# Kernel optimization log

Hardware: AMD Instinct MI355X
Metric: run time of the kernel (lower is better)

The kernel has to match this reference:

```python
import jax, jax.numpy as jnp
import numpy as np

IMG_H, IMG_W = 800, 1216
STRIDE = 16
SIZES = (128.0, 256.0, 512.0)
RATIOS = (0.5, 1.0, 2.0)
NMS_THRESH = 0.7
MIN_SIZE = 16.0
PRE_NMS = 6000   # testing mode
POST_NMS = 300   # testing mode


def _base_anchors():
    # torchvision-style: ratio = h/w, anchors centered at origin, xyxy
    base = []
    for s in SIZES:
        for r in RATIOS:
            hr = np.sqrt(r)
            w, h = s / hr, s * hr
            base.append([-w / 2.0, -h / 2.0, w / 2.0, h / 2.0])
    return jnp.asarray(np.array(base, dtype=np.float32))  # [A,4]


def _anchors(H, W):
    base = _base_anchors()                                  # [A,4]
    sx = jnp.arange(W, dtype=jnp.float32) * STRIDE
    sy = jnp.arange(H, dtype=jnp.float32) * STRIDE
    shift_x, shift_y = jnp.meshgrid(sx, sy)                 # [H,W] each
    shifts = jnp.stack([shift_x, shift_y, shift_x, shift_y], axis=-1)
    # row-major over (h, w), anchors innermost -> matches permute(0,2,3,1) layout
    return (shifts.reshape(-1, 1, 4) + base[None]).reshape(-1, 4)  # [H*W*A,4]


def _conv(x, w, b, pad):
    y = jax.lax.conv_general_dilated(x, w, (1, 1), pad,
                                     dimension_numbers=('NCHW', 'OIHW', 'NCHW'))
    return y + b[None, :, None, None]


def _decode(deltas, anchors):
    wa = anchors[:, 2] - anchors[:, 0]
    ha = anchors[:, 3] - anchors[:, 1]
    cxa = anchors[:, 0] + 0.5 * wa
    cya = anchors[:, 1] + 0.5 * ha
    cx = deltas[:, 0] * wa + cxa
    cy = deltas[:, 1] * ha + cya
    w = jnp.exp(deltas[:, 2]) * wa
    h = jnp.exp(deltas[:, 3]) * ha
    return jnp.stack([cx - 0.5 * w, cy - 0.5 * h, cx + 0.5 * w, cy + 0.5 * h], axis=-1)


def _nms(boxes, scores):
    # boxes: [N,4] sorted by descending score; greedy IoU-suppression NMS
    N = boxes.shape[0]
    areas = (boxes[:, 2] - boxes[:, 0]) * (boxes[:, 3] - boxes[:, 1])

    def body(i, st):
        sup, kidx, kval = st
        avail = jnp.where(sup, -jnp.inf, scores)
        j = jnp.argmax(avail)
        valid = avail[j] > -jnp.inf
        b = boxes[j]
        ix1 = jnp.maximum(b[0], boxes[:, 0])
        iy1 = jnp.maximum(b[1], boxes[:, 1])
        ix2 = jnp.minimum(b[2], boxes[:, 2])
        iy2 = jnp.minimum(b[3], boxes[:, 3])
        inter = jnp.clip(ix2 - ix1, 0.0) * jnp.clip(iy2 - iy1, 0.0)
        union = areas[j] + areas - inter
        iou = jnp.where(union > 0, inter / union, 0.0)
        sup2 = (sup | (iou > NMS_THRESH)).at[j].set(True)
        sup = jnp.where(valid, sup2, sup.at[j].set(True))
        return sup, kidx.at[i].set(j), kval.at[i].set(valid)

    sup0 = jnp.zeros((N,), jnp.bool_)
    _, kidx, kval = jax.lax.fori_loop(
        0, POST_NMS, body,
        (sup0, jnp.zeros((POST_NMS,), jnp.int32), jnp.zeros((POST_NMS,), jnp.bool_)))
    # fixed-size output [POST_NMS,4]; invalid slots zeroed
    return boxes[kidx] * kval[:, None].astype(boxes.dtype)


def setup_inputs() -> dict:
    key = jax.random.key(0)
    ks = jax.random.split(key, 4)
    return {
        'features': jax.random.normal(ks[0], (8, 512, 50, 76), jnp.float32),
        'conv_w': 0.01 * jax.random.normal(ks[1], (512, 512, 3, 3), jnp.float32),
        'conv_b': jnp.zeros((512,), jnp.float32),
        'cls_w': 0.01 * jax.random.normal(ks[2], (9, 512, 1, 1), jnp.float32),
        'cls_b': jnp.zeros((9,), jnp.float32),
        'box_w': 0.01 * jax.random.normal(ks[3], (36, 512, 1, 1), jnp.float32),
        'box_b': jnp.zeros((36,), jnp.float32),
    }


def reference(features, conv_w, conv_b, cls_w, cls_b, box_w, box_b):
    B, _, H, W = features.shape
    t = jax.nn.relu(_conv(features, conv_w, conv_b, 'SAME'))
    obj = _conv(t, cls_w, cls_b, 'VALID')                     # [B,A,H,W]
    objectness = jnp.transpose(obj, (0, 2, 3, 1)).reshape(B, -1)        # [B,N]
    bd = _conv(t, box_w, box_b, 'VALID')                      # [B,4A,H,W]
    bbox_deltas = jnp.transpose(bd, (0, 2, 3, 1)).reshape(B, -1, 4)     # [B,N,4]
    anchors = _anchors(H, W)                                  # [N,4]

    def per_image(scores, deltas):
        props = _decode(deltas, anchors)
        props = jnp.stack([jnp.clip(props[:, 0], 0.0, IMG_W),
                           jnp.clip(props[:, 1], 0.0, IMG_H),
                           jnp.clip(props[:, 2], 0.0, IMG_W),
                           jnp.clip(props[:, 3], 0.0, IMG_H)], axis=-1)
        keep = ((props[:, 2] - props[:, 0]) >= MIN_SIZE) & \
               ((props[:, 3] - props[:, 1]) >= MIN_SIZE)
        s = jnp.where(keep, scores, -jnp.inf)  # small boxes never selected
        top_s, top_i = jax.lax.top_k(s, PRE_NMS)
        return _nms(props[top_i], top_s)

    proposals = jax.vmap(per_image)(objectness, bbox_deltas)  # [B,POST_NMS,4]
    return proposals, objectness, bbox_deltas
```

## Files before the change

### kernel.cpp

```cpp
#include <hip/hip_runtime.h>
#include <stdint.h>
#include <math.h>

typedef unsigned int u32;
typedef unsigned long long u64;
typedef double d4 __attribute__((ext_vector_type(4)));
typedef _Float16 h8 __attribute__((ext_vector_type(8)));
typedef float f32x16 __attribute__((ext_vector_type(16)));

#define NPX    3800
#define NANCH  34200
#define NSEL   6000
#define NOUT   300
#define NPXP   4160

#define OFF_T        0ull
#define OFF_WTH      62259200ull
#define OFF_WTL      66977792ull
#define OFF_BOXES    71696384ull
#define OFF_ITEMS    76073984ull
#define OFF_FSPH     78262784ull
#define OFF_FSPL     112341504ull
#define WS_NEED_F16  146551296ull
#define OFF_PART     OFF_FSPH
#define WS_NEED_SPLITK (OFF_PART + 43776000ull)

#define GLL16(gsrc, ldst) \
    __builtin_amdgcn_global_load_lds((const __attribute__((address_space(1))) void*)(gsrc), \
                                     (__attribute__((address_space(3))) void*)(ldst), 16, 0, 0)

__global__ __launch_bounds__(256) void zero_kernel(float4* __restrict__ p, unsigned n) {
    unsigned i = blockIdx.x * 256u + threadIdx.x;
    const unsigned stride = gridDim.x * 256u;
    const float4 z = make_float4(0.f, 0.f, 0.f, 0.f);
    for (; i < n; i += stride) p[i] = z;
}

__global__ __launch_bounds__(256) void wsplit_kernel(const float* __restrict__ cw,
                                                     _Float16* __restrict__ wh,
                                                     _Float16* __restrict__ wl) {
    int o = blockIdx.x * 256 + threadIdx.x;
    if (o >= 9 * 512 * 512) return;
    int ci = o & 511;
    int co = (o >> 9) & 511;
    int kk = o >> 18;
    float v = cw[(((co << 9) + ci) * 9) + kk] * 1024.0f;
    _Float16 h = (_Float16)v;
    float r = v - (float)h;
    wh[o] = h;
    wl[o] = (_Float16)r;
}

__global__ __launch_bounds__(256) void fsplit_kernel(const float* __restrict__ feat,
                                                     _Float16* __restrict__ fh,
                                                     _Float16* __restrict__ fl) {
    const int b = blockIdx.z, ci0 = blockIdx.y << 5, p0 = blockIdx.x << 6;
    const int tid = threadIdx.x;
    __shared__ __align__(16) _Float16 shh[64][32];
    __shared__ __align__(16) _Float16 shl[64][32];
    {
        const int r = tid >> 3, xg = tid & 7;
        const int p = p0 + (xg << 3);
        float v[8];
        if (p < NPX) {
            const float* sp = feat + ((size_t)(b * 512 + ci0 + r)) * NPX + p;
            #pragma unroll
            for (int j = 0; j < 8; ++j) v[j] = sp[j];
        } else {
            #pragma unroll
            for (int j = 0; j < 8; ++j) v[j] = 0.f;
        }
        #pragma unroll
        for (int j = 0; j < 8; ++j) {
            float s = v[j] * 512.0f;
            _Float16 h = (_Float16)s;
            float rr = s - (float)h;
            shh[(xg << 3) + j][r] = h;
            shl[(xg << 3) + j][r] = (_Float16)rr;
        }
    }
    __syncthreads();
    {
        const int px = tid >> 2, cg = tid & 3;
        const int p = p0 + px;
        if (p < NPX) {
            const int yy = p / 76, xx = p - yy * 76;
            const size_t dst = ((size_t)b * NPXP + (size_t)((yy + 1) * 80 + xx + 2)) * 512
                             + ci0 + (cg << 3);
            *(h8*)(fh + dst) = *(const h8*)&shh[px][cg << 3];
            *(h8*)(fl + dst) = *(const h8*)&shl[px][cg << 3];
        }
    }
}

__global__ __launch_bounds__(512, 2) void conv3x3_f16_kernel(
    const _Float16* __restrict__ fh, const _Float16* __restrict__ fl,
    const _Float16* __restrict__ wh, const _Float16* __restrict__ wl,
    const float* __restrict__ bias, float* __restrict__ t)
{
    const int id  = blockIdx.x;
    const int b   = id & 7;
    const int g   = id >> 3;
    const int co0 = (g >> 4) << 7;
    const int pt0 = (g & 15) << 8;
    const int tid = threadIdx.x;
    const int w   = tid >> 6;
    const int l   = tid & 63;
    const int wm  = w >> 2, wn = w & 3;
    const int ln  = l & 31, lk = l >> 5;

    __shared__ __align__(16) _Float16 S[5][24][512];

    const _Float16* sb[3];
    u32 ldof[3];
    bool isA[3];
    const long long fbase = (long long)b * NPXP + pt0;
    #pragma unroll
    for (int i = 0; i < 3; ++i) {
        const int ti = w * 3 + i;
        ldof[i] = (u32)(ti * 1024 + l * 16);
        isA[i] = (ti < 8);
        if (ti < 8) {
            const int mt = ti >> 1, hl = ti & 1;
            sb[i] = (hl ? wl : wh) + ((long long)(co0 + (mt << 5) + ln) << 9) + (lk << 3);
        } else {
            const int tj = ti - 8, nt = tj >> 1, hl = tj & 1;
            sb[i] = (hl ? fl : fh) + ((fbase + (nt << 5) + ln) << 9) + (lk << 3);
        }
    }
    char* lbase = (char*)&S[0][0][0];

    auto stage = [&](int q, int slot) {
        const int kk  = q >> 5;
        const int ci0 = (q & 31) << 4;
        const long long offA = ((long long)kk << 18) + ci0;
        const int kd = (kk * 11) >> 5;
        const int s  = kd * 77 + kk - 81;
        const long long offB = ((long long)s << 9) + ci0;
        char* ld = lbase + slot * 24576;
        #pragma unroll
        for (int i = 0; i < 3; ++i) {
            const long long off = isA[i] ? offA : offB;
            GLL16(sb[i] + off, ld + ldof[i]);
        }
    };

    f32x16 acc[2][2], l2[2][2];
    #pragma unroll
    for (int i = 0; i < 2; ++i)
        #pragma unroll
        for (int j = 0; j < 2; ++j)
            #pragma unroll
            for (int gg = 0; gg < 16; ++gg) { acc[i][j][gg] = 0.0f; l2[i][j][gg] = 0.0f; }

    const int ao = l << 3;

    auto readFrags = [&](int slot, h8* Ah, h8* Al, h8* Bh, h8* Bl) {
        const _Float16* Sq = (const _Float16*)(lbase + slot * 24576);
        #pragma unroll
        for (int i = 0; i < 2; ++i) {
            const int mt = (wm << 1) + i, nt = (wn << 1) + i;
            Ah[i] = *(const h8*)(Sq + (((mt << 1) + 0) << 9) + ao);
            Al[i] = *(const h8*)(Sq + (((mt << 1) + 1) << 9) + ao);
            Bh[i] = *(const h8*)(Sq + ((8 + (nt << 1) + 0) << 9) + ao);
            Bl[i] = *(const h8*)(Sq + ((8 + (nt << 1) + 1) << 9) + ao);
        }
    };

    stage(0, 0); stage(1, 1); stage(2, 2);
    asm volatile("s_waitcnt vmcnt(3)" ::: "memory");
    __builtin_amdgcn_sched_barrier(0);
    __builtin_amdgcn_s_barrier();

    int s0 = 0;
    for (int F = 0; F < 144; ++F) {
        const int q0 = F << 1;
        int s1 = s0 + 1; if (s1 >= 5) s1 -= 5;
        int s3 = s0 + 3; if (s3 >= 5) s3 -= 5;
        int s4 = s0 + 4; if (s4 >= 5) s4 -= 5;
        if (q0 + 3 < 288) stage(q0 + 3, s3);
        if (q0 + 4 < 288) stage(q0 + 4, s4);

        h8 A0h[2], A0l[2], B0h[2], B0l[2];
        h8 A1h[2], A1l[2], B1h[2], B1l[2];
        readFrags(s0, A0h, A0l, B0h, B0l);
        __builtin_amdgcn_s_setprio(1);
        acc[0][0] = __builtin_amdgcn_mfma_f32_32x32x16_f16(A0h[0], B0h[0], acc[0][0], 0, 0, 0);
        acc[0][0] = __builtin_amdgcn_mfma_f32_32x32x16_f16(A0h[0], B0l[0], acc[0][0], 0, 0, 0);
        acc[0][0] = __builtin_amdgcn_mfma_f32_32x32x16_f16(A0l[0], B0h[0], acc[0][0], 0, 0, 0);
        acc[0][1] = __builtin_amdgcn_mfma_f32_32x32x16_f16(A0h[0], B0h[1], acc[0][1], 0, 0, 0);
        acc[0][1] = __builtin_amdgcn_mfma_f32_32x32x16_f16(A0h[0], B0l[1], acc[0][1], 0, 0, 0);
        acc[0][1] = __builtin_amdgcn_mfma_f32_32x32x16_f16(A0l[0], B0h[1], acc[0][1], 0, 0, 0);
        __builtin_amdgcn_s_setprio(0);
        readFrags(s1, A1h, A1l, B1h, B1l);
        __builtin_amdgcn_s_setprio(1);
        acc[1][0] = __builtin_amdgcn_mfma_f32_32x32x16_f16(A0h[1], B0h[0], acc[1][0], 0, 0, 0);
        acc[1][0] = __builtin_amdgcn_mfma_f32_32x32x16_f16(A0h[1], B0l[0], acc[1][0], 0, 0, 0);
        acc[1][0] = __builtin_amdgcn_mfma_f32_32x32x16_f16(A0l[1], B0h[0], acc[1][0], 0, 0, 0);
        acc[1][1] = __builtin_amdgcn_mfma_f32_32x32x16_f16(A0h[1], B0h[1], acc[1][1], 0, 0, 0);
        acc[1][1] = __builtin_amdgcn_mfma_f32_32x32x16_f16(A0h[1], B0l[1], acc[1][1], 0, 0, 0);
        acc[1][1] = __builtin_amdgcn_mfma_f32_32x32x16_f16(A0l[1], B0h[1], acc[1][1], 0, 0, 0);
        acc[0][0] = __builtin_amdgcn_mfma_f32_32x32x16_f16(A1h[0], B1h[0], acc[0][0], 0, 0, 0);
        acc[0][0] = __builtin_amdgcn_mfma_f32_32x32x16_f16(A1h[0], B1l[0], acc[0][0], 0, 0, 0);
        acc[0][0] = __builtin_amdgcn_mfma_f32_32x32x16_f16(A1l[0], B1h[0], acc[0][0], 0, 0, 0);
        acc[0][1] = __builtin_amdgcn_mfma_f32_32x32x16_f16(A1h[0], B1h[1], acc[0][1], 0, 0, 0);
        acc[0][1] = __builtin_amdgcn_mfma_f32_32x32x16_f16(A1h[0], B1l[1], acc[0][1], 0, 0, 0);
        acc[0][1] = __builtin_amdgcn_mfma_f32_32x32x16_f16(A1l[0], B1h[1], acc[0][1], 0, 0, 0);
        acc[1][0] = __builtin_amdgcn_mfma_f32_32x32x16_f16(A1h[1], B1h[0], acc[1][0], 0, 0, 0);
        acc[1][0] = __builtin_amdgcn_mfma_f32_32x32x16_f16(A1h[1], B1l[0], acc[1][0], 0, 0, 0);
        acc[1][0] = __builtin_amdgcn_mfma_f32_32x32x16_f16(A1l[1], B1h[0], acc[1][0], 0, 0, 0);
        acc[1][1] = __builtin_amdgcn_mfma_f32_32x32x16_f16(A1h[1], B1h[1], acc[1][1], 0, 0, 0);
        acc[1][1] = __builtin_amdgcn_mfma_f32_32x32x16_f16(A1h[1], B1l[1], acc[1][1], 0, 0, 0);
        acc[1][1] = __builtin_amdgcn_mfma_f32_32x32x16_f16(A1l[1], B1h[1], acc[1][1], 0, 0, 0);
        __builtin_amdgcn_s_setprio(0);

        if (((q0 + 1) & 7) == 7) {
            #pragma unroll
            for (int i = 0; i < 2; ++i)
                #pragma unroll
                for (int j = 0; j < 2; ++j) {
                    l2[i][j] += acc[i][j];
                    #pragma unroll
                    for (int gg = 0; gg < 16; ++gg) acc[i][j][gg] = 0.0f;
                }
        }

        if (F < 143) {
            if (q0 + 4 < 288) { asm volatile("s_waitcnt vmcnt(3)" ::: "memory"); }
            else              { asm volatile("s_waitcnt vmcnt(0)" ::: "memory"); }
            __builtin_amdgcn_sched_barrier(0);
            __builtin_amdgcn_s_barrier();
        }
        s0 += 2; if (s0 >= 5) s0 -= 5;
    }

    int rcp[16];
    {
        h8 pa, pb;
        #pragma unroll
        for (int j = 0; j < 8; ++j) { pa[j] = (_Float16)(float)ln; pb[j] = (_Float16)0.0625f; }
        f32x16 pr, pc;
        #pragma unroll
        for (int gg = 0; gg < 16; ++gg) { pr[gg] = 0.0f; pc[gg] = 0.0f; }
        pr = __builtin_amdgcn_mfma_f32_32x32x16_f16(pa, pb, pr, 0, 0, 0);
        pc = __builtin_amdgcn_mfma_f32_32x32x16_f16(pb, pa, pc, 0, 0, 0);
        #pragma unroll
        for (int gg = 0; gg < 16; ++gg)
            rcp[gg] = ((int)(pr[gg] + 0.5f)) | (((int)(pc[gg] + 0.5f)) << 8);
    }

    const double dsc = 1.0 / 524288.0;
    #pragma unroll
    for (int i = 0; i < 2; ++i) {
        #pragma unroll
        for (int j = 0; j < 2; ++j) {
            #pragma unroll
            for (int gg = 0; gg < 16; ++gg) {
                const int row = rcp[gg] & 255;
                const int col = rcp[gg] >> 8;
                const int co  = co0 + (wm << 6) + (i << 5) + row;
                const int pp  = pt0 + (wn << 6) + (j << 5) + col;
                const int yy  = pp / 80;
                const int xx  = pp - yy * 80;
                if (yy >= 1 && yy < 51 && xx >= 2 && xx < 78) {
                    const double v = (double)l2[i][j][gg] * dsc + (double)bias[co];
                    t[((size_t)(b * 512 + co)) * NPX + (yy - 1) * 76 + (xx - 2)]
                        = (float)(v > 0.0 ? v : 0.0);
                }
            }
        }
    }
}

__global__ __launch_bounds__(1024) void wtrans_kernel(const float* __restrict__ cw,
                                                      float* __restrict__ wt) {
    int o = blockIdx.x * 1024 + threadIdx.x;
    if (o >= 512*512*9) return;
    int co = o & 511;
    int ci = (o >> 9) & 511;
    int kk = o >> 18;
    wt[o] = cw[((co << 9) + ci) * 9 + kk];
}

__global__ __launch_bounds__(256, 2) void conv3x3_mfma_kernel(const float* __restrict__ feat,
                                                              const float* __restrict__ wt,
                                                              const float* __restrict__ bias,
                                                              float* __restrict__ t) {
    const int b   = blockIdx.z;
    const int co0 = blockIdx.y << 7;
    const int px0 = blockIdx.x << 6;
    const int tid = threadIdx.x;
    const int w    = tid >> 6;
    const int l    = tid & 63;
    const int quad = l >> 4;
    const int lc   = l & 15;

    __shared__ double BsF[2][1024];

    int rr[4], cc[4];
    {
        d4 pzr = {0.0, 0.0, 0.0, 0.0};
        d4 pzc = {0.0, 0.0, 0.0, 0.0};
        double paM = (double)lc;
        double pbN = (double)lc;
        pzr = __builtin_amdgcn_mfma_f64_16x16x4f64(paM, 1.0, pzr, 0, 0, 0);
        pzc = __builtin_amdgcn_mfma_f64_16x16x4f64(1.0, pbN, pzc, 0, 0, 0);
        #pragma unroll
        for (int g = 0; g < 4; ++g) {
            rr[g] = (((int)pzr[g]) >> 2) & 15;
            cc[g] = (((int)pzc[g]) >> 2) & 15;
        }
    }

    d4 acc[2][4];
    #pragma unroll
    for (int i = 0; i < 2; ++i)
        #pragma unroll
        for (int j = 0; j < 4; ++j) acc[i][j] = (d4){0.0, 0.0, 0.0, 0.0};

    const float* featb = feat + (size_t)b * 512 * NPX;

    const int b_quad = (tid >> 4) & 3;
    const int b_pxl  = ((tid >> 6) << 4) | (tid & 15);
    const int p      = px0 + b_pxl;
    const int py     = p / 76;
    const int px     = p - py * 76;
    const bool pvalid = (p < NPX);

    float vaf[8], vbf[4];
    double a_cur[8];

    auto loadA = [&](int q, float* va) {
        int kk  = q >> 5;
        int ci0 = (q & 31) << 4;
        const float* ap = wt + (((size_t)(kk * 512 + ci0 + quad)) << 9)
                             + co0 + (w << 5) + lc;
        #pragma unroll
        for (int ks = 0; ks < 4; ++ks) {
            va[ks * 2 + 0] = ap[(ks << 11)];
            va[ks * 2 + 1] = ap[(ks << 11) + 16];
        }
    };
    auto loadB = [&](int q, float* vb) {
        int kk  = q >> 5;
        int ci0 = (q & 31) << 4;
        int kd = kk / 3;
        int dy = kd - 1, dx = kk - kd * 3 - 1;
        int iy = py + dy, ix = px + dx;
        bool ok = pvalid && ((unsigned)iy < 50u) && ((unsigned)ix < 76u);
        if (ok) {
            const float* bp = featb + (size_t)(ci0 + b_quad) * NPX + iy * 76 + ix;
            #pragma unroll
            for (int j = 0; j < 4; ++j) vb[j] = bp[(size_t)(j << 2) * NPX];
        } else {
            vb[0] = vb[1] = vb[2] = vb[3] = 0.0f;
        }
    };

    loadA(0, vaf); loadB(0, vbf);
    #pragma unroll
    for (int j = 0; j < 4; ++j) BsF[0][tid + (j << 8)] = (double)vbf[j];
    #pragma unroll
    for (int j = 0; j < 8; ++j) a_cur[j] = (double)vaf[j];
    __syncthreads();

    for (int q = 0; q < 288; ++q) {
        const int cur = q & 1;
        if (q < 287) { loadA(q + 1, vaf); loadB(q + 1, vbf); }
        const double* bb = BsF[cur];
        #pragma unroll
        for (int ks = 0; ks < 4; ++ks) {
            const double* bp = bb + (ks << 8);
            double a0 = a_cur[ks * 2], a1 = a_cur[ks * 2 + 1];
            #pragma unroll
            for (int nt = 0; nt < 4; ++nt) {
                double bv = bp[(nt << 6) + l];
                acc[0][nt] = __builtin_amdgcn_mfma_f64_16x16x4f64(a0, bv, acc[0][nt], 0, 0, 0);
                acc[1][nt] = __builtin_amdgcn_mfma_f64_16x16x4f64(a1, bv, acc[1][nt], 0, 0, 0);
            }
        }
        if (q < 287) {
            #pragma unroll
            for (int j = 0; j < 4; ++j) BsF[cur ^ 1][tid + (j << 8)] = (double)vbf[j];
            #pragma unroll
            for (int j = 0; j < 8; ++j) a_cur[j] = (double)vaf[j];
            __syncthreads();
        }
    }

    #pragma unroll
    for (int mt = 0; mt < 2; ++mt) {
        #pragma unroll
        for (int g = 0; g < 4; ++g) {
            int co = co0 + (w << 5) + (mt << 4) + rr[g];
            double bs = (double)bias[co];
            float* row = t + ((size_t)b * 512 + co) * NPX;
            #pragma unroll
            for (int nt = 0; nt < 4; ++nt) {
                int pp = px0 + (nt << 4) + cc[g];
                if (pp < NPX) {
                    double v = acc[mt][nt][g] + bs;
                    row[pp] = (float)(v > 0.0 ? v : 0.0);
                }
            }
        }
    }
}

__global__ __launch_bounds__(64) void heads_partial_kernel(const float* __restrict__ t,
                                                           const float* __restrict__ cls_w,
                                                           const float* __restrict__ box_w,
                                                           double* __restrict__ part) {
    const int b = blockIdx.y, c = blockIdx.z;
    const int p = blockIdx.x * 64 + threadIdx.x;
    if (p >= NPX) return;
    const float* tb = t + ((size_t)b * 512 + c * 128) * NPX + p;

    double ac[9]  = {};
    double ab[36] = {};
    for (int ci = 0; ci < 128; ++ci) {
        double tv = (double)tb[(size_t)ci * NPX];
        int cw = c * 128 + ci;
        #pragma unroll
        for (int o = 0; o < 9;  ++o) ac[o] = fma((double)cls_w[o * 512 + cw], tv, ac[o]);
        #pragma unroll
        for (int o = 0; o < 36; ++o) ab[o] = fma((double)box_w[o * 512 + cw], tv, ab[o]);
    }
    double* dst = part + ((size_t)(c * 8 + b) * 45) * NPX + p;
    #pragma unroll
    for (int o = 0; o < 9;  ++o) dst[(size_t)o * NPX] = ac[o];
    #pragma unroll
    for (int o = 0; o < 36; ++o) dst[(size_t)(9 + o) * NPX] = ab[o];
}

__device__ __forceinline__ void decode_px(int b, int p, const double* s45,
                                          const float* cls_b, const float* box_b,
                                          float* out_obj, float* out_del,
                                          float* boxes, u64* items) {
    float* ob = out_obj + (size_t)b * NANCH + (size_t)p * 9;
    float* dl = out_del + (size_t)b * NANCH * 4 + (size_t)p * 36;
    const int yy = p / 76, xx = p - yy * 76;

    #pragma unroll
    for (int a = 0; a < 9; ++a) {
        double s  = s45[a] + (double)cls_b[a];
        ob[a] = (float)s;
        double d0 = s45[9 + 4*a + 0] + (double)box_b[4*a+0];
        double d1 = s45[9 + 4*a + 1] + (double)box_b[4*a+1];
        double d2 = s45[9 + 4*a + 2] + (double)box_b[4*a+2];
        double d3 = s45[9 + 4*a + 3] + (double)box_b[4*a+3];
        dl[4*a+0] = (float)d0; dl[4*a+1] = (float)d1;
        dl[4*a+2] = (float)d2; dl[4*a+3] = (float)d3;

        int si = a / 3, ri = a - si * 3;
        double sz = (si == 0) ? 128.0 : ((si == 1) ? 256.0 : 512.0);
        double hr = (ri == 0) ? 0.7071067811865476 : ((ri == 1) ? 1.0 : 1.4142135623730951);
        float bx2f = (float)(sz / hr * 0.5);
        float by2f = (float)(sz * hr * 0.5);

        double sx = (double)(xx * 16), sy = (double)(yy * 16);
        double x1 = sx - (double)bx2f, x2 = sx + (double)bx2f;
        double y1 = sy - (double)by2f, y2 = sy + (double)by2f;

        double wa = x2 - x1, ha = y2 - y1;
        double cxa = x1 + 0.5 * wa, cya = y1 + 0.5 * ha;
        double cx = d0 * wa + cxa, cy = d1 * ha + cya;
        double w  = exp(d2) * wa,  h  = exp(d3) * ha;

        double px1 = cx - 0.5 * w, py1 = cy - 0.5 * h;
        double px2 = cx + 0.5 * w, py2 = cy + 0.5 * h;
        px1 = fmin(fmax(px1, 0.0), 1216.0);
        py1 = fmin(fmax(py1, 0.0), 800.0);
        px2 = fmin(fmax(px2, 0.0), 1216.0);
        py2 = fmin(fmax(py2, 0.0), 800.0);

        bool keep = ((px2 - px1) >= 16.0) && ((py2 - py1) >= 16.0);
        double se = keep ? s : -INFINITY;

        u64 ubits = (u64)__double_as_longlong(se);
        u64 ka = (ubits >> 63) ? ~ubits : (ubits | 0x8000000000000000ull);
        u64 kd = ~ka;
        int n = p * 9 + a;
        items[(size_t)b * NANCH + n] = (kd & ~0xFFFFull) | (u64)(u32)n;
        *(float4*)(boxes + ((size_t)b * NANCH + n) * 4) =
            make_float4((float)px1, (float)py1, (float)px2, (float)py2);
    }
}

__global__ __launch_bounds__(64) void reduce_decode_kernel(const double* __restrict__ part,
                                                           const float* __restrict__ cls_b,
                                                           const float* __restrict__ box_b,
                                                           float* __restrict__ out_obj,
                                                           float* __restrict__ out_del,
                                                           float* __restrict__ boxes,
                                                           u64* __restrict__ items) {
    const int b = blockIdx.y;
    const int p = blockIdx.x * 64 + threadIdx.x;
    if (p >= NPX) return;
    double s45[45];
    #pragma unroll
    for (int o = 0; o < 45; ++o) {
        double s = part[((size_t)(0 * 8 + b) * 45 + o) * NPX + p];
        s += part[((size_t)(1 * 8 + b) * 45 + o) * NPX + p];
        s += part[((size_t)(2 * 8 + b) * 45 + o) * NPX + p];
        s += part[((size_t)(3 * 8 + b) * 45 + o) * NPX + p];
        s45[o] = s;
    }
    decode_px(b, p, s45, cls_b, box_b, out_obj, out_del, boxes, items);
}

__global__ __launch_bounds__(256) void heads_decode_kernel(const float* __restrict__ t,
                                                           const float* __restrict__ cls_w,
                                                           const float* __restrict__ cls_b,
                                                           const float* __restrict__ box_w,
                                                           const float* __restrict__ box_b,
                                                           float* __restrict__ out_obj,
                                                           float* __restrict__ out_del,
                                                           float* __restrict__ boxes,
                                                           u64* __restrict__ items) {
    const int b = blockIdx.y;
    const int p = blockIdx.x * 256 + threadIdx.x;
    if (p >= NPX) return;
    const float* tb = t + (size_t)b * 512 * NPX + p;
    double s45[45];
    #pragma unroll
    for (int o = 0; o < 45; ++o) s45[o] = 0.0;
    for (int ci = 0; ci < 512; ++ci) {
        double tv = (double)tb[(size_t)ci * NPX];
        #pragma unroll
        for (int o = 0; o < 9;  ++o) s45[o]     = fma((double)cls_w[o * 512 + ci], tv, s45[o]);
        #pragma unroll
        for (int o = 0; o < 36; ++o) s45[9 + o] = fma((double)box_w[o * 512 + ci], tv, s45[9 + o]);
    }
    decode_px(b, p, s45, cls_b, box_b, out_obj, out_del, boxes, items);
}

__device__ __forceinline__ bool iou_gt(float4 A, float4 B, float areaA, float areaB) {
    float ix1 = fmaxf(A.x, B.x), iy1 = fmaxf(A.y, B.y);
    float ix2 = fminf(A.z, B.z), iy2 = fminf(A.w, B.w);
    float iw = fmaxf(ix2 - ix1, 0.0f), ih = fmaxf(iy2 - iy1, 0.0f);
    float inter = iw * ih;
    float uni = areaA + areaB - inter;
    float iou = (uni > 0.0f) ? (inter / uni) : 0.0f;
    return iou > 0.7f;
}

__global__ __launch_bounds__(1024) void topk_nms_kernel(const u64* __restrict__ items,
                                                        const float* __restrict__ boxes,
                                                        float* __restrict__ out) {
    extern __shared__ u64 buf[];
    u32* hist = (u32*)buf;
    u32* scan = hist + 4096;
    u32* scal = hist + 5120;

    const int b   = blockIdx.x;
    const int tid = threadIdx.x;
    const u64* it = items + (size_t)b * NANCH;

    #pragma unroll
    for (int i = 0; i < 4; ++i) hist[tid * 4 + i] = 0;
    __syncthreads();
    for (int i = tid; i < NANCH; i += 1024)
        atomicAdd(&hist[(u32)(it[i] >> 52)], 1);
    __syncthreads();

    u32 B1, cum1;
    {
        u32 c0 = hist[tid*4], c1 = hist[tid*4+1], c2 = hist[tid*4+2], c3 = hist[tid*4+3];
        u32 S = c0 + c1 + c2 + c3;
        scan[tid] = S;
        __syncthreads();
        for (int off = 1; off < 1024; off <<= 1) {
            u32 v = (tid >= off) ? scan[tid - off] : 0;
            __syncthreads();
            scan[tid] += v;
            __syncthreads();
        }
        u32 excl = scan[tid] - S;
        const u32 target = 5999;
        if (target >= excl && target < excl + S) {
            u32 pfx = excl, bidx, cum;
            if      (target < pfx + c0)           { bidx = tid*4;   cum = pfx; }
            else if (target < pfx + c0 + c1)      { bidx = tid*4+1; cum = pfx + c0; }
            else if (target < pfx + c0 + c1 + c2) { bidx = tid*4+2; cum = pfx + c0 + c1; }
            else                                  { bidx = tid*4+3; cum = pfx + c0 + c1 + c2; }
            scal[0] = bidx; scal[1] = cum;
        }
    }
    __syncthreads();
    B1 = scal[0]; cum1 = scal[1];
    __syncthreads();

    #pragma unroll
    for (int i = 0; i < 4; ++i) hist[tid * 4 + i] = 0;
    __syncthreads();
    for (int i = tid; i < NANCH; i += 1024) {
        u64 v = it[i];
        if ((u32)(v >> 52) == B1)
            atomicAdd(&hist[(u32)(v >> 40) & 0xFFF], 1);
    }
    __syncthreads();

    u32 B2;
    {
        u32 c0 = hist[tid*4], c1 = hist[tid*4+1], c2 = hist[tid*4+2], c3 = hist[tid*4+3];
        u32 S = c0 + c1 + c2 + c3;
        scan[tid] = S;
        __syncthreads();
        for (int off = 1; off < 1024; off <<= 1) {
            u32 v = (tid >= off) ? scan[tid - off] : 0;
            __syncthreads();
            scan[tid] += v;
            __syncthreads();
        }
        u32 excl = scan[tid] - S;
        const u32 target = 5999 - cum1;
        if (target >= excl && target < excl + S) {
            u32 pfx = excl, bidx;
            if      (target < pfx + c0)           bidx = tid*4;
            else if (target < pfx + c0 + c1)      bidx = tid*4+1;
            else if (target < pfx + c0 + c1 + c2) bidx = tid*4+2;
            else                                  bidx = tid*4+3;
            scal[2] = bidx;
        }
    }
    __syncthreads();
    B2 = scal[2];
    const u32 T = ((B1 << 12) | B2) + 1;
    __syncthreads();

    for (int i = tid; i < 8192; i += 1024) buf[i] = ~0ull;
    __syncthreads();
    u32* cnt = (u32*)&buf[8191];
    if (tid == 0) *cnt = 0;
    __syncthreads();
    for (int i = tid; i < NANCH; i += 1024) {
        u64 v = it[i];
        if ((u32)(v >> 40) < T) {
            u32 pos = atomicAdd(cnt, 1);
            if (pos < 8191) buf[pos] = v;
        }
    }
    __syncthreads();
    if (tid == 0) buf[8191] = ~0ull;
    __syncthreads();

    for (int size = 2; size <= 8192; size <<= 1) {
        for (int stride = size >> 1; stride > 0; stride >>= 1) {
            #pragma unroll
            for (int v = 0; v < 4; ++v) {
                int idx = tid + (v << 10);
                int i = 2 * idx - (idx & (stride - 1));
                int j = i + stride;
                bool up = ((i & size) == 0);
                u64 x = buf[i], y = buf[j];
                if ((x > y) == up) { buf[i] = y; buf[j] = x; }
            }
            __syncthreads();
        }
    }

    float4 bx6[6]; u32 dead6[6];
    #pragma unroll
    for (int s = 0; s < 6; ++s) {
        int r = tid + (s << 10);
        u64 v = buf[r];
        bool dd = (r >= NSEL) || ((u32)(v >> 32) >= 0xFFF00000u);
        float4 bb = make_float4(0.f, 0.f, 0.f, 0.f);
        if (!dd) {
            u32 n = (u32)(v & 0xFFFFull);
            bb = *(const float4*)(boxes + ((size_t)b * NANCH + n) * 4);
        }
        bx6[s] = bb;
        dead6[s] = dd ? 1u : 0u;
    }
    __syncthreads();

    float4* candbox = (float4*)buf;
    u64*    wmask   = (u64*)(buf + 2560);
    float4* accb    = (float4*)(buf + 3072);
    u32*    cntp    = (u32*)(buf + 3712);
    if (tid == 0) *cntp = 0;
    __syncthreads();

    for (int s = 0; s < 6; ++s) {
        int count = (int)*cntp;
        if (count >= NOUT) break;
        float4 mb = bx6[s];
        float  ma = (mb.z - mb.x) * (mb.w - mb.y);
        bool dd = dead6[s] != 0;
        for (int a2 = 0; a2 < count && !dd; ++a2) {
            float4 abx = accb[a2];
            if (iou_gt(mb, abx, ma, (abx.z - abx.x) * (abx.w - abx.y))) dd = true;
        }
        candbox[tid] = mb;
        u64 bal = __ballot(!dd);
        if ((tid & 63) == 0) wmask[tid >> 6] = bal;
        __syncthreads();
        if (tid < 64) {
            int cnt2 = count;
            for (int w2 = 0; w2 < 16 && cnt2 < NOUT; ++w2) {
                u64 mm = wmask[w2];
                while (mm != 0 && cnt2 < NOUT) {
                    int bit = __ffsll(mm) - 1;
                    mm &= (mm - 1);
                    float4 cb = candbox[(w2 << 6) + bit];
                    float  ca = (cb.z - cb.x) * (cb.w - cb.y);
                    bool okc = true;
                    for (int base = count; base < cnt2 && okc; base += 64) {
                        int idx = base + tid;
                        bool bad = false;
                        if (idx < cnt2) {
                            float4 abx = accb[idx];
                            bad = iou_gt(cb, abx, ca, (abx.z - abx.x) * (abx.w - abx.y));
                        }
                        if (__any(bad)) okc = false;
                    }
                    if (okc) {
                        if (tid == 0) accb[cnt2] = cb;
                        cnt2++;
                    }
                }
            }
            if (tid == 0) *cntp = (u32)cnt2;
        }
        __syncthreads();
    }

    int fin = (int)*cntp;
    for (int r = tid; r < NOUT; r += 1024) {
        float4 v = (r < fin) ? accb[r] : make_float4(0.f, 0.f, 0.f, 0.f);
        *(float4*)(out + ((size_t)b * NOUT + r) * 4) = v;
    }
}

extern "C" void kernel_launch(void* const* d_in, const int* in_sizes, int n_in,
                              void* d_out, int out_size, void* d_ws, size_t ws_size,
                              hipStream_t stream) {
    const float* feat   = (const float*)d_in[0];
    const float* conv_w = (const float*)d_in[1];
    const float* conv_b = (const float*)d_in[2];
    const float* cls_w  = (const float*)d_in[3];
    const float* cls_b  = (const float*)d_in[4];
    const float* box_w  = (const float*)d_in[5];
    const float* box_b  = (const float*)d_in[6];

    float* out       = (float*)d_out;
    float* out_props = out;
    float* out_obj   = out + 9600;
    float* out_del   = out + 9600 + 273600;

    char* ws = (char*)d_ws;
    float*    t     = (float*)(ws + OFF_T);
    _Float16* wth   = (_Float16*)(ws + OFF_WTH);
    _Float16* wtl   = (_Float16*)(ws + OFF_WTL);
    float*    wtf   = (float*)(ws + OFF_WTH);
    float*    boxes = (float*)(ws + OFF_BOXES);
    u64*      items = (u64*)(ws + OFF_ITEMS);
    _Float16* fsph  = (_Float16*)(ws + OFF_FSPH);
    _Float16* fspl  = (_Float16*)(ws + OFF_FSPL);
    double*   part  = (double*)(ws + OFF_PART);

    if (ws_size >= WS_NEED_F16) {
        hipLaunchKernelGGL(zero_kernel, dim3(2048), dim3(256), 0, stream,
                           (float4*)(ws + OFF_FSPH), 4259840u);
        hipLaunchKernelGGL(wsplit_kernel, dim3(9216), dim3(256), 0, stream,
                           conv_w, wth, wtl);
        hipLaunchKernelGGL(fsplit_kernel, dim3(60, 16, 8), dim3(256), 0, stream,
                           feat, fsph, fspl);
        hipLaunchKernelGGL(conv3x3_f16_kernel, dim3(512), dim3(512), 0, stream,
                           fsph, fspl, wth, wtl, conv_b, t);
    } else {
        hipLaunchKernelGGL(wtrans_kernel, dim3(2304), dim3(1024), 0, stream, conv_w, wtf);
        hipLaunchKernelGGL(conv3x3_mfma_kernel, dim3(60, 4, 8), dim3(256), 0, stream,
                           feat, wtf, conv_b, t);
    }
    if (ws_size >= WS_NEED_SPLITK) {
        hipLaunchKernelGGL(heads_partial_kernel, dim3(60, 8, 4), dim3(64), 0, stream,
                           t, cls_w, box_w, part);
        hipLaunchKernelGGL(reduce_decode_kernel, dim3(60, 8), dim3(64), 0, stream,
                           part, cls_b, box_b, out_obj, out_del, boxes, items);
    } else {
        hipLaunchKernelGGL(heads_decode_kernel, dim3(15, 8), dim3(256), 0, stream,
                           t, cls_w, cls_b, box_w, box_b, out_obj, out_del, boxes, items);
    }
    hipLaunchKernelGGL(topk_nms_kernel, dim3(8), dim3(1024), 65536, stream,
                       items, boxes, out_props);
}
```

Before: 1.130 ms.

## Fuse prep kernels with halo-only zeroing and software-pipeline MFMA fragment reads

The zero, weight-split and feature-split kernels are merged into one prep kernel. It zeroes only the padded halo border instead of the whole padded feature buffers, which removes two launches and most of the zero-fill traffic. In the conv main loop, LDS fragment reads are pipelined one step ahead so MFMAs on the previous fragments overlap the next reads. The loop now waits with vmcnt(0) instead of vmcnt(3), which may expose global-load latency more often.

```diff
diff --git a/kernel.cpp b/kernel.cpp
--- a/kernel.cpp
+++ b/kernel.cpp
@@ -29,66 +29,82 @@
     __builtin_amdgcn_global_load_lds((const __attribute__((address_space(1))) void*)(gsrc), \
                                      (__attribute__((address_space(3))) void*)(ldst), 16, 0, 0)
 
-__global__ __launch_bounds__(256) void zero_kernel(float4* __restrict__ p, unsigned n) {
-    unsigned i = blockIdx.x * 256u + threadIdx.x;
-    const unsigned stride = gridDim.x * 256u;
-    const float4 z = make_float4(0.f, 0.f, 0.f, 0.f);
-    for (; i < n; i += stride) p[i] = z;
-}
-
-__global__ __launch_bounds__(256) void wsplit_kernel(const float* __restrict__ cw,
-                                                     _Float16* __restrict__ wh,
-                                                     _Float16* __restrict__ wl) {
-    int o = blockIdx.x * 256 + threadIdx.x;
-    if (o >= 9 * 512 * 512) return;
-    int ci = o & 511;
-    int co = (o >> 9) & 511;
-    int kk = o >> 18;
-    float v = cw[(((co << 9) + ci) * 9) + kk] * 1024.0f;
-    _Float16 h = (_Float16)v;
-    float r = v - (float)h;
-    wh[o] = h;
-    wl[o] = (_Float16)r;
-}
-
-__global__ __launch_bounds__(256) void fsplit_kernel(const float* __restrict__ feat,
-                                                     _Float16* __restrict__ fh,
-                                                     _Float16* __restrict__ fl) {
-    const int b = blockIdx.z, ci0 = blockIdx.y << 5, p0 = blockIdx.x << 6;
+__global__ __launch_bounds__(256) void prep_kernel(const float* __restrict__ feat,
+                                                   const float* __restrict__ cw,
+                                                   _Float16* __restrict__ wh,
+                                                   _Float16* __restrict__ wl,
+                                                   _Float16* __restrict__ fh,
+                                                   _Float16* __restrict__ fl) {
+    const int bid = blockIdx.x;
     const int tid = threadIdx.x;
     __shared__ __align__(16) _Float16 shh[64][32];
     __shared__ __align__(16) _Float16 shl[64][32];
-    {
-        const int r = tid >> 3, xg = tid & 7;
-        const int p = p0 + (xg << 3);
-        float v[8];
-        if (p < NPX) {
-            const float* sp = feat + ((size_t)(b * 512 + ci0 + r)) * NPX + p;
-            #pragma unroll
-            for (int j = 0; j < 8; ++j) v[j] = sp[j];
-        } else {
-            #pragma unroll
-            for (int j = 0; j < 8; ++j) v[j] = 0.f;
-        }
-        #pragma unroll
-        for (int j = 0; j < 8; ++j) {
-            float s = v[j] * 512.0f;
-            _Float16 h = (_Float16)s;
-            float rr = s - (float)h;
-            shh[(xg << 3) + j][r] = h;
-            shl[(xg << 3) + j][r] = (_Float16)rr;
-        }
-    }
-    __syncthreads();
-    {
-        const int px = tid >> 2, cg = tid & 3;
-        const int p = p0 + px;
-        if (p < NPX) {
-            const int yy = p / 76, xx = p - yy * 76;
-            const size_t dst = ((size_t)b * NPXP + (size_t)((yy + 1) * 80 + xx + 2)) * 512
-                             + ci0 + (cg << 3);
-            *(h8*)(fh + dst) = *(const h8*)&shh[px][cg << 3];
-            *(h8*)(fl + dst) = *(const h8*)&shl[px][cg << 3];
+
+    if (bid < 9216) {
+        int o = bid * 256 + tid;
+        int ci = o & 511;
+        int co = (o >> 9) & 511;
+        int kk = o >> 18;
+        float v = cw[(((co << 9) + ci) * 9) + kk] * 1024.0f;
+        _Float16 h = (_Float16)v;
+        float r = v - (float)h;
+        wh[o] = h;
+        wl[o] = (_Float16)r;
+    } else if (bid < 9216 + 7680) {
+        int idx = bid - 9216;
+        const int pb = idx % 60; idx /= 60;
+        const int b  = idx >> 4;
+        const int ci0 = (idx & 15) << 5;
+        const int p0  = pb << 6;
+        {
+            const int r = tid >> 3, xg = tid & 7;
+            const int p = p0 + (xg << 3);
+            float v[8];
+            if (p < NPX) {
+                const float* sp = feat + ((size_t)(b * 512 + ci0 + r)) * NPX + p;
+                #pragma unroll
+                for (int j = 0; j < 8; ++j) v[j] = sp[j];
+            } else {
+                #pragma unroll
+                for (int j = 0; j < 8; ++j) v[j] = 0.f;
+            }
+            #pragma unroll
+            for (int j = 0; j < 8; ++j) {
+                float s = v[j] * 512.0f;
+                _Float16 h = (_Float16)s;
+                float rr = s - (float)h;
+                shh[(xg << 3) + j][r] = h;
+                shl[(xg << 3) + j][r] = (_Float16)rr;
+            }
+        }
+        __syncthreads();
+        {
+            const int px = tid >> 2, cg = tid & 3;
+            const int p = p0 + px;
+            if (p < NPX) {
+                const int yy = p / 76, xx = p - yy * 76;
+                const size_t dst = ((size_t)b * NPXP + (size_t)((yy + 1) * 80 + xx + 2)) * 512
+                                 + ci0 + (cg << 3);
+                *(h8*)(fh + dst) = *(const h8*)&shh[px][cg << 3];
+                *(h8*)(fl + dst) = *(const h8*)&shl[px][cg << 3];
+            }
+        }
+    } else {
+        int idx = (bid - 16896) * 256 + tid;
+        int task = idx >> 2, sub = idx & 3;
+        if (task < 2880) {
+            int b = task / 360, c = task - b * 360;
+            int yp, xp;
+            if      (c < 80)  { yp = 0;  xp = c; }
+            else if (c < 160) { yp = 51; xp = c - 80; }
+            else { int c2 = c - 160; yp = 1 + (c2 >> 2); int m = c2 & 3; xp = (m < 2) ? m : (76 + m); }
+            const size_t base = ((size_t)b * NPXP + (size_t)(yp * 80 + xp)) * 512 + sub * 128;
+            h8 z = {};
+            #pragma unroll
+            for (int j = 0; j < 16; ++j) {
+                *(h8*)(fh + base + (j << 3)) = z;
+                *(h8*)(fl + base + (j << 3)) = z;
+            }
         }
     }
 }
@@ -168,38 +184,45 @@
     };
 
     stage(0, 0); stage(1, 1); stage(2, 2);
-    asm volatile("s_waitcnt vmcnt(3)" ::: "memory");
+    asm volatile("s_waitcnt vmcnt(0)" ::: "memory");
     __builtin_amdgcn_sched_barrier(0);
     __builtin_amdgcn_s_barrier();
+    __builtin_amdgcn_sched_barrier(0);
+
+    h8 PAh[2], PAl[2], PBh[2], PBl[2];
+    readFrags(0, PAh, PAl, PBh, PBl);
 
     int s0 = 0;
     for (int F = 0; F < 144; ++F) {
         const int q0 = F << 1;
         int s1 = s0 + 1; if (s1 >= 5) s1 -= 5;
+        int s2 = s0 + 2; if (s2 >= 5) s2 -= 5;
         int s3 = s0 + 3; if (s3 >= 5) s3 -= 5;
         int s4 = s0 + 4; if (s4 >= 5) s4 -= 5;
         if (q0 + 3 < 288) stage(q0 + 3, s3);
         if (q0 + 4 < 288) stage(q0 + 4, s4);
 
-        h8 A0h[2], A0l[2], B0h[2], B0l[2];
         h8 A1h[2], A1l[2], B1h[2], B1l[2];
-        readFrags(s0, A0h, A0l, B0h, B0l);
+        readFrags(s1, A1h, A1l, B1h, B1l);
+
         __builtin_amdgcn_s_setprio(1);
-        acc[0][0] = __builtin_amdgcn_mfma_f32_32x32x16_f16(A0h[0], B0h[0], acc[0][0], 0, 0, 0);
-        acc[0][0] = __builtin_amdgcn_mfma_f32_32x32x16_f16(A0h[0], B0l[0], acc[0][0], 0, 0, 0);
-        acc[0][0] = __builtin_amdgcn_mfma_f32_32x32x16_f16(A0l[0], B0h[0], acc[0][0], 0, 0, 0);
-        acc[0][1] = __builtin_amdgcn_mfma_f32_32x32x16_f16(A0h[0], B0h[1], acc[0][1], 0, 0, 0);
-        acc[0][1] = __builtin_amdgcn_mfma_f32_32x32x16_f16(A0h[0], B0l[1], acc[0][1], 0, 0, 0);
-        acc[0][1] = __builtin_amdgcn_mfma_f32_32x32x16_f16(A0l[0], B0h[1], acc[0][1], 0, 0, 0);
+        acc[0][0] = __builtin_amdgcn_mfma_f32_32x32x16_f16(PAh[0], PBh[0], acc[0][0], 0, 0, 0);
+        acc[0][0] = __builtin_amdgcn_mfma_f32_32x32x16_f16(PAh[0], PBl[0], acc[0][0], 0, 0, 0);
+        acc[0][0] = __builtin_amdgcn_mfma_f32_32x32x16_f16(PAl[0], PBh[0], acc[0][0], 0, 0, 0);
+        acc[0][1] = __builtin_amdgcn_mfma_f32_32x32x16_f16(PAh[0], PBh[1], acc[0][1], 0, 0, 0);
+        acc[0][1] = __builtin_amdgcn_mfma_f32_32x32x16_f16(PAh[0], PBl[1], acc[0][1], 0, 0, 0);
+        acc[0][1] = __builtin_amdgcn_mfma_f32_32x32x16_f16(PAl[0], PBh[1], acc[0][1], 0, 0, 0);
+        acc[1][0] = __builtin_amdgcn_mfma_f32_32x32x16_f16(PAh[1], PBh[0], acc[1][0], 0, 0, 0);
+        acc[1][0] = __builtin_amdgcn_mfma_f32_32x32x16_f16(PAh[1], PBl[0], acc[1][0], 0, 0, 0);
+        acc[1][0] = __builtin_amdgcn_mfma_f32_32x32x16_f16(PAl[1], PBh[0], acc[1][0], 0, 0, 0);
+        acc[1][1] = __builtin_amdgcn_mfma_f32_32x32x16_f16(PAh[1], PBh[1], acc[1][1], 0, 0, 0);
+        acc[1][1] = __builtin_amdgcn_mfma_f32_32x32x16_f16(PAh[1], PBl[1], acc[1][1], 0, 0, 0);
+        acc[1][1] = __builtin_amdgcn_mfma_f32_32x32x16_f16(PAl[1], PBh[1], acc[1][1], 0, 0, 0);
         __builtin_amdgcn_s_setprio(0);
-        readFrags(s1, A1h, A1l, B1h, B1l);
+
+        if (F < 143) readFrags(s2, PAh, PAl, PBh, PBl);
+
         __builtin_amdgcn_s_setprio(1);
-        acc[1][0] = __builtin_amdgcn_mfma_f32_32x32x16_f16(A0h[1], B0h[0], acc[1][0], 0, 0, 0);
-        acc[1][0] = __builtin_amdgcn_mfma_f32_32x32x16_f16(A0h[1], B0l[0], acc[1][0], 0, 0, 0);
-        acc[1][0] = __builtin_amdgcn_mfma_f32_32x32x16_f16(A0l[1], B0h[0], acc[1][0], 0, 0, 0);
-        acc[1][1] = __builtin_amdgcn_mfma_f32_32x32x16_f16(A0h[1], B0h[1], acc[1][1], 0, 0, 0);
-        acc[1][1] = __builtin_amdgcn_mfma_f32_32x32x16_f16(A0h[1], B0l[1], acc[1][1], 0, 0, 0);
-        acc[1][1] = __builtin_amdgcn_mfma_f32_32x32x16_f16(A0l[1], B0h[1], acc[1][1], 0, 0, 0);
         acc[0][0] = __builtin_amdgcn_mfma_f32_32x32x16_f16(A1h[0], B1h[0], acc[0][0], 0, 0, 0);
         acc[0][0] = __builtin_amdgcn_mfma_f32_32x32x16_f16(A1h[0], B1l[0], acc[0][0], 0, 0, 0);
         acc[0][0] = __builtin_amdgcn_mfma_f32_32x32x16_f16(A1l[0], B1h[0], acc[0][0], 0, 0, 0);
@@ -226,10 +249,11 @@
         }
 
         if (F < 143) {
-            if (q0 + 4 < 288) { asm volatile("s_waitcnt vmcnt(3)" ::: "memory"); }
-            else              { asm volatile("s_waitcnt vmcnt(0)" ::: "memory"); }
+            __builtin_amdgcn_sched_barrier(0);
+            asm volatile("s_waitcnt vmcnt(0)" ::: "memory");
             __builtin_amdgcn_sched_barrier(0);
             __builtin_amdgcn_s_barrier();
+            __builtin_amdgcn_sched_barrier(0);
         }
         s0 += 2; if (s0 >= 5) s0 -= 5;
     }
@@ -762,12 +786,8 @@
     double*   part  = (double*)(ws + OFF_PART);
 
     if (ws_size >= WS_NEED_F16) {
-        hipLaunchKernelGGL(zero_kernel, dim3(2048), dim3(256), 0, stream,
-                           (float4*)(ws + OFF_FSPH), 4259840u);
-        hipLaunchKernelGGL(wsplit_kernel, dim3(9216), dim3(256), 0, stream,
-                           conv_w, wth, wtl);
-        hipLaunchKernelGGL(fsplit_kernel, dim3(60, 16, 8), dim3(256), 0, stream,
-                           feat, fsph, fspl);
+        hipLaunchKernelGGL(prep_kernel, dim3(16941), dim3(256), 0, stream,
+                           feat, conv_w, wth, wtl, fsph, fspl);
         hipLaunchKernelGGL(conv3x3_f16_kernel, dim3(512), dim3(512), 0, stream,
                            fsph, fspl, wth, wtl, conv_b, t);
     } else {
```

Result: slower. 1.154 ms (+2.1%).
